# Performance work log

Measured on AMD Instinct MI355X. Metric: run time of the kernel, lower is better.

The kernel has to match this reference:

```python
import jax, jax.numpy as jnp
import numpy as np

BATCH, N_CTX, N_TGT = 4096, 8, 16
NUM_DOCS, NUM_WORDS, VEC_DIM = 500, 8000, 128


def setup_inputs() -> dict:
    key = jax.random.key(0)
    k1, k2, k3, k4, k5, k6 = jax.random.split(key, 6)
    context_ids = jax.random.randint(k1, (BATCH, N_CTX), 0, NUM_WORDS, dtype=jnp.int64 if jax.config.jax_enable_x64 else jnp.int32)
    doc_ids = jax.random.randint(k2, (BATCH,), 0, NUM_DOCS, dtype=context_ids.dtype)
    target_noise_ids = jax.random.randint(k3, (BATCH, N_TGT), 0, NUM_WORDS, dtype=context_ids.dtype)
    D = jax.random.normal(k4, (NUM_DOCS, NUM_WORDS, VEC_DIM), dtype=jnp.float32)
    W = jax.random.normal(k5, (NUM_WORDS, VEC_DIM), dtype=jnp.float32)
    O = jax.random.normal(k6, (VEC_DIM, NUM_WORDS), dtype=jnp.float32)
    return {"context_ids": context_ids, "doc_ids": doc_ids,
            "target_noise_ids": target_noise_ids, "D": D, "W": W, "O": O}


def reference(context_ids, doc_ids, target_noise_ids, D, W, O):
    # Gather per-(doc, context-word) vectors: (B, C, V)
    d_vecs = D[doc_ids[:, None], context_ids, :]
    # Add global word vectors and sum over context dim -> (B, V)
    x = jnp.sum(d_vecs + W[context_ids, :], axis=1)
    # Gather output columns per sample: O.T[target_noise_ids] -> (B, T, V)
    o_vecs = O.T[target_noise_ids]
    # Batched dot product -> (B, T) scores
    result = jnp.einsum('bv,btv->bt', x, o_vecs)
    return result
```

## Files before the change

### kernel.cpp

```cpp
#include <hip/hip_runtime.h>

#define BATCH     4096
#define N_CTX     8
#define N_TGT     16
#define NUM_DOCS  500
#define NUM_WORDS 8000
#define VEC_DIM   128

__global__ __launch_bounds__(256) void transpose_O_kernel(
    const float* __restrict__ O, float* __restrict__ OT) {
  __shared__ float tile[32][33];
  const int wBase = blockIdx.x * 32;
  const int vBase = blockIdx.y * 32;
  const int tx = threadIdx.x;
  const int ty = threadIdx.y;
#pragma unroll
  for (int i = ty; i < 32; i += 8) {
    tile[i][tx] = O[(size_t)(vBase + i) * NUM_WORDS + (wBase + tx)];
  }
  __syncthreads();
#pragma unroll
  for (int i = ty; i < 32; i += 8) {
    OT[(size_t)(wBase + i) * VEC_DIM + (vBase + tx)] = tile[tx][i];
  }
}

__global__ __launch_bounds__(256, 2) void fused_kernel(
    const int* __restrict__ ctx, const int* __restrict__ docs,
    const int* __restrict__ tgt, const float* __restrict__ D,
    const float* __restrict__ W, const float* __restrict__ OT,
    float* __restrict__ out) {
  const int wave = threadIdx.x >> 6;
  const int lane = threadIdx.x & 63;
  const int hl   = lane & 31;
  const int b = (blockIdx.x * 4 + wave) * 2 + (lane >> 5);

  const int4 c0 = *(const int4*)(ctx + b * N_CTX);
  const int4 c1 = *(const int4*)(ctx + b * N_CTX + 4);
  const int  doc = docs[b];
  const int4 t0 = *(const int4*)(tgt + b * N_TGT);
  const int4 t1 = *(const int4*)(tgt + b * N_TGT + 4);
  const int4 t2 = *(const int4*)(tgt + b * N_TGT + 8);
  const int4 t3 = *(const int4*)(tgt + b * N_TGT + 12);
  const int cw[N_CTX] = {c0.x, c0.y, c0.z, c0.w, c1.x, c1.y, c1.z, c1.w};
  const int tw[N_TGT] = {t0.x, t0.y, t0.z, t0.w, t1.x, t1.y, t1.z, t1.w,
                         t2.x, t2.y, t2.z, t2.w, t3.x, t3.y, t3.z, t3.w};

  const float* Dbase = D + (size_t)doc * (NUM_WORDS * VEC_DIM) + 4 * hl;
  const float* Wbase = W + 4 * hl;
  const float* Obase = OT + 4 * hl;

  float4 o[N_TGT];
#pragma unroll
  for (int t = 0; t < N_TGT; ++t)
    o[t] = *(const float4*)(Obase + (size_t)tw[t] * VEC_DIM);

  float4 acc = make_float4(0.f, 0.f, 0.f, 0.f);
#pragma unroll
  for (int c = 0; c < N_CTX; ++c) {
    const float4 d = *(const float4*)(Dbase + (size_t)cw[c] * VEC_DIM);
    const float4 w = *(const float4*)(Wbase + (size_t)cw[c] * VEC_DIM);
    acc.x += d.x + w.x;
    acc.y += d.y + w.y;
    acc.z += d.z + w.z;
    acc.w += d.w + w.w;
  }

  float p[N_TGT];
#pragma unroll
  for (int t = 0; t < N_TGT; ++t)
    p[t] = acc.x * o[t].x + acc.y * o[t].y + acc.z * o[t].z + acc.w * o[t].w;

  const bool h4 = (lane & 16) != 0;
  float q[8];
#pragma unroll
  for (int t = 0; t < 8; ++t) {
    const float send = h4 ? p[t] : p[t + 8];
    const float recv = __shfl_xor(send, 16, 64);
    q[t] = (h4 ? p[t + 8] : p[t]) + recv;
  }
  const bool h3 = (lane & 8) != 0;
  float r[4];
#pragma unroll
  for (int t = 0; t < 4; ++t) {
    const float send = h3 ? q[t] : q[t + 4];
    const float recv = __shfl_xor(send, 8, 64);
    r[t] = (h3 ? q[t + 4] : q[t]) + recv;
  }
  const bool h2 = (lane & 4) != 0;
  float s2[2];
#pragma unroll
  for (int t = 0; t < 2; ++t) {
    const float send = h2 ? r[t] : r[t + 2];
    const float recv = __shfl_xor(send, 4, 64);
    s2[t] = (h2 ? r[t + 2] : r[t]) + recv;
  }
  const bool h1 = (lane & 2) != 0;
  float u;
  {
    const float send = h1 ? s2[0] : s2[1];
    const float recv = __shfl_xor(send, 2, 64);
    u = (h1 ? s2[1] : s2[0]) + recv;
  }
  u += __shfl_xor(u, 1, 64);

  if ((lane & 1) == 0) out[b * N_TGT + ((hl >> 1) & 15)] = u;
}

extern "C" void kernel_launch(void* const* d_in, const int* in_sizes, int n_in,
                              void* d_out, int out_size, void* d_ws, size_t ws_size,
                              hipStream_t stream) {
  const int*   ctx  = (const int*)d_in[0];
  const int*   docs = (const int*)d_in[1];
  const int*   tgt  = (const int*)d_in[2];
  const float* D    = (const float*)d_in[3];
  const float* W    = (const float*)d_in[4];
  const float* O    = (const float*)d_in[5];
  float*       out  = (float*)d_out;

  float* OT = (float*)d_ws;
  transpose_O_kernel<<<dim3(NUM_WORDS / 32, VEC_DIM / 32), dim3(32, 8), 0, stream>>>(O, OT);
  fused_kernel<<<dim3(BATCH / 8), dim3(256), 0, stream>>>(ctx, docs, tgt, D, W, OT, out);
}
```

Baseline: 20.22 us.

## Overlap O transpose with context gather in first kernel, dot in second

New measurement: 19.07 us. 5.7% less time.

```diff
diff --git a/kernel.cpp b/kernel.cpp
--- a/kernel.cpp
+++ b/kernel.cpp
@@ -6,70 +6,107 @@
 #define NUM_DOCS  500
 #define NUM_WORDS 8000
 #define VEC_DIM   128
+#define N_TILES   ((NUM_WORDS / 32) * (VEC_DIM / 32))
 
-__global__ __launch_bounds__(256) void transpose_O_kernel(
-    const float* __restrict__ O, float* __restrict__ OT) {
-  __shared__ float tile[32][33];
-  const int wBase = blockIdx.x * 32;
-  const int vBase = blockIdx.y * 32;
-  const int tx = threadIdx.x;
-  const int ty = threadIdx.y;
+typedef float floatx4 __attribute__((ext_vector_type(4)));
+
+__global__ __launch_bounds__(256, 2) void k1_gather_transpose(
+    const int* __restrict__ ctx, const int* __restrict__ docs,
+    const float* __restrict__ D, const float* __restrict__ W,
+    const float* __restrict__ O, float* __restrict__ OT,
+    float* __restrict__ X) {
+  const int tid  = threadIdx.x;
+  const int wave = tid >> 6;
+  const int lane = tid & 63;
+  const int hl   = lane & 31;
+  const int b = (blockIdx.x * 4 + wave) * 2 + (lane >> 5);
+
+  __shared__ float tile[2][32][33];
+  const int tx = tid & 31;
+  const int ty = tid >> 5;
+
+  float r[2][4];
+  int wB[2], vB[2], tok[2];
 #pragma unroll
-  for (int i = ty; i < 32; i += 8) {
-    tile[i][tx] = O[(size_t)(vBase + i) * NUM_WORDS + (wBase + tx)];
+  for (int s = 0; s < 2; ++s) {
+    const int ti = blockIdx.x * 2 + s;
+    tok[s] = (ti < N_TILES);
+    wB[s] = (ti % (NUM_WORDS / 32)) * 32;
+    vB[s] = (ti / (NUM_WORDS / 32)) * 32;
+    if (tok[s]) {
+#pragma unroll
+      for (int i = 0; i < 4; ++i)
+        r[s][i] = O[(size_t)(vB[s] + ty + 8 * i) * NUM_WORDS + (wB[s] + tx)];
+    }
+  }
+
+  const int4 c0 = *(const int4*)(ctx + b * N_CTX);
+  const int4 c1 = *(const int4*)(ctx + b * N_CTX + 4);
+  const int  doc = docs[b];
+  const int cw[N_CTX] = {c0.x, c0.y, c0.z, c0.w, c1.x, c1.y, c1.z, c1.w};
+  const float* Dbase = D + (size_t)doc * (NUM_WORDS * VEC_DIM) + 4 * hl;
+  const float* Wbase = W + 4 * hl;
+  floatx4 dd[N_CTX], ww[N_CTX];
+#pragma unroll
+  for (int c = 0; c < N_CTX; ++c) {
+    dd[c] = __builtin_nontemporal_load(
+        (const floatx4*)(Dbase + (size_t)cw[c] * VEC_DIM));
+    ww[c] = *(const floatx4*)(Wbase + (size_t)cw[c] * VEC_DIM);
+  }
+
+#pragma unroll
+  for (int s = 0; s < 2; ++s) {
+    if (tok[s]) {
+#pragma unroll
+      for (int i = 0; i < 4; ++i) tile[s][ty + 8 * i][tx] = r[s][i];
+    }
   }
   __syncthreads();
 #pragma unroll
-  for (int i = ty; i < 32; i += 8) {
-    OT[(size_t)(wBase + i) * VEC_DIM + (vBase + tx)] = tile[tx][i];
+  for (int s = 0; s < 2; ++s) {
+    if (tok[s]) {
+#pragma unroll
+      for (int i = 0; i < 4; ++i)
+        OT[(size_t)(wB[s] + ty + 8 * i) * VEC_DIM + (vB[s] + tx)] =
+            tile[s][tx][ty + 8 * i];
+    }
   }
+
+  floatx4 acc = {0.f, 0.f, 0.f, 0.f};
+#pragma unroll
+  for (int c = 0; c < N_CTX; ++c) acc += dd[c] + ww[c];
+  *(floatx4*)(X + (size_t)b * VEC_DIM + 4 * hl) = acc;
 }
 
-__global__ __launch_bounds__(256, 2) void fused_kernel(
-    const int* __restrict__ ctx, const int* __restrict__ docs,
-    const int* __restrict__ tgt, const float* __restrict__ D,
-    const float* __restrict__ W, const float* __restrict__ OT,
-    float* __restrict__ out) {
+__global__ __launch_bounds__(256, 2) void k2_dot(
+    const int* __restrict__ tgt, const float* __restrict__ X,
+    const float* __restrict__ OT, float* __restrict__ out) {
   const int wave = threadIdx.x >> 6;
   const int lane = threadIdx.x & 63;
   const int hl   = lane & 31;
   const int b = (blockIdx.x * 4 + wave) * 2 + (lane >> 5);
 
-  const int4 c0 = *(const int4*)(ctx + b * N_CTX);
-  const int4 c1 = *(const int4*)(ctx + b * N_CTX + 4);
-  const int  doc = docs[b];
   const int4 t0 = *(const int4*)(tgt + b * N_TGT);
   const int4 t1 = *(const int4*)(tgt + b * N_TGT + 4);
   const int4 t2 = *(const int4*)(tgt + b * N_TGT + 8);
   const int4 t3 = *(const int4*)(tgt + b * N_TGT + 12);
-  const int cw[N_CTX] = {c0.x, c0.y, c0.z, c0.w, c1.x, c1.y, c1.z, c1.w};
   const int tw[N_TGT] = {t0.x, t0.y, t0.z, t0.w, t1.x, t1.y, t1.z, t1.w,
                          t2.x, t2.y, t2.z, t2.w, t3.x, t3.y, t3.z, t3.w};
 
-  const float* Dbase = D + (size_t)doc * (NUM_WORDS * VEC_DIM) + 4 * hl;
-  const float* Wbase = W + 4 * hl;
   const float* Obase = OT + 4 * hl;
-
-  float4 o[N_TGT];
+  floatx4 o[N_TGT];
 #pragma unroll
   for (int t = 0; t < N_TGT; ++t)
-    o[t] = *(const float4*)(Obase + (size_t)tw[t] * VEC_DIM);
+    o[t] = *(const floatx4*)(Obase + (size_t)tw[t] * VEC_DIM);
 
-  float4 acc = make_float4(0.f, 0.f, 0.f, 0.f);
-#pragma unroll
-  for (int c = 0; c < N_CTX; ++c) {
-    const float4 d = *(const float4*)(Dbase + (size_t)cw[c] * VEC_DIM);
-    const float4 w = *(const float4*)(Wbase + (size_t)cw[c] * VEC_DIM);
-    acc.x += d.x + w.x;
-    acc.y += d.y + w.y;
-    acc.z += d.z + w.z;
-    acc.w += d.w + w.w;
-  }
+  const floatx4 xv = *(const floatx4*)(X + (size_t)b * VEC_DIM + 4 * hl);
 
   float p[N_TGT];
 #pragma unroll
-  for (int t = 0; t < N_TGT; ++t)
-    p[t] = acc.x * o[t].x + acc.y * o[t].y + acc.z * o[t].z + acc.w * o[t].w;
+  for (int t = 0; t < N_TGT; ++t) {
+    const floatx4 m = xv * o[t];
+    p[t] = m.x + m.y + m.z + m.w;
+  }
 
   const bool h4 = (lane & 16) != 0;
   float q[8];
@@ -80,20 +117,20 @@
     q[t] = (h4 ? p[t + 8] : p[t]) + recv;
   }
   const bool h3 = (lane & 8) != 0;
-  float r[4];
+  float rr[4];
 #pragma unroll
   for (int t = 0; t < 4; ++t) {
     const float send = h3 ? q[t] : q[t + 4];
     const float recv = __shfl_xor(send, 8, 64);
-    r[t] = (h3 ? q[t + 4] : q[t]) + recv;
+    rr[t] = (h3 ? q[t + 4] : q[t]) + recv;
   }
   const bool h2 = (lane & 4) != 0;
   float s2[2];
 #pragma unroll
   for (int t = 0; t < 2; ++t) {
-    const float send = h2 ? r[t] : r[t + 2];
+    const float send = h2 ? rr[t] : rr[t + 2];
     const float recv = __shfl_xor(send, 4, 64);
-    s2[t] = (h2 ? r[t + 2] : r[t]) + recv;
+    s2[t] = (h2 ? rr[t + 2] : rr[t]) + recv;
   }
   const bool h1 = (lane & 2) != 0;
   float u;
@@ -119,6 +156,9 @@
   float*       out  = (float*)d_out;
 
   float* OT = (float*)d_ws;
-  transpose_O_kernel<<<dim3(NUM_WORDS / 32, VEC_DIM / 32), dim3(32, 8), 0, stream>>>(O, OT);
-  fused_kernel<<<dim3(BATCH / 8), dim3(256), 0, stream>>>(ctx, docs, tgt, D, W, OT, out);
+  float* X  = (float*)d_ws + (size_t)NUM_WORDS * VEC_DIM;
+
+  k1_gather_transpose<<<dim3(BATCH / 8), dim3(256), 0, stream>>>(
+      ctx, docs, D, W, O, OT, X);
+  k2_dot<<<dim3(BATCH / 8), dim3(256), 0, stream>>>(tgt, X, OT, out);
 }
```
